# Performance work log

Hardware: AMD Instinct MI355X
Metric: run time of the kernel (lower is better)

## Reference

```python
import jax, jax.numpy as jnp
import numpy as np

N = 50000
E = 800000
F_IN = 128
HID = 64
HEADS = 4
EPS_BN = 1e-5
NEG_SLOPE = 0.2


def setup_inputs() -> dict:
    key = jax.random.key(0)
    ks = jax.random.split(key, 20)
    s = 0.05
    d = {
        "x": jax.random.normal(ks[0], (N, F_IN), jnp.float32),
        "edge_index": jax.random.randint(ks[1], (2, E), 0, N, dtype=jnp.int32),
        # layer 0: F_IN -> HID x HEADS (concat)
        "W0": jax.random.normal(ks[2], (F_IN, HEADS * HID), jnp.float32) * s,
        "as0": jax.random.normal(ks[3], (HEADS, HID), jnp.float32) * s,
        "ad0": jax.random.normal(ks[4], (HEADS, HID), jnp.float32) * s,
        "b0": jnp.zeros((HEADS * HID,), jnp.float32),
        # layer 1: HEADS*HID -> HID (heads=1)
        "W1": jax.random.normal(ks[5], (HEADS * HID, HID), jnp.float32) * s,
        "as1": jax.random.normal(ks[6], (1, HID), jnp.float32) * s,
        "ad1": jax.random.normal(ks[7], (1, HID), jnp.float32) * s,
        "b1": jnp.zeros((HID,), jnp.float32),
        # layer 2: HID -> HID (heads=1)
        "W2": jax.random.normal(ks[8], (HID, HID), jnp.float32) * s,
        "as2": jax.random.normal(ks[9], (1, HID), jnp.float32) * s,
        "ad2": jax.random.normal(ks[10], (1, HID), jnp.float32) * s,
        "b2": jnp.zeros((HID,), jnp.float32),
        # MLP head
        "lw1": jax.random.normal(ks[11], (HID, HID), jnp.float32) * s,
        "lb1": jnp.zeros((HID,), jnp.float32),
        "lw2": jax.random.normal(ks[12], (HID, 2), jnp.float32) * s,
        "lb2": jnp.zeros((2,), jnp.float32),
    }
    return d


def batch_norm(x):
    # track_running_stats=False, affine=False: per-batch stats, biased var
    mu = jnp.mean(x, axis=0)
    var = jnp.mean((x - mu) ** 2, axis=0)
    return (x - mu) / jnp.sqrt(var + EPS_BN)


def gat_conv(x, src, dst, W, att_src, att_dst, bias, heads, out_dim):
    n = x.shape[0]
    h = (x @ W).reshape(n, heads, out_dim)            # [N,H,D]
    a_src = jnp.sum(h * att_src, axis=-1)             # [N,H]
    a_dst = jnp.sum(h * att_dst, axis=-1)             # [N,H]
    e = a_src[src] + a_dst[dst]                       # [E',H]
    e = jax.nn.leaky_relu(e, NEG_SLOPE)
    # softmax over incoming edges of each destination node
    m = jax.ops.segment_max(e, dst, num_segments=n)   # [N,H]
    e = jnp.exp(e - m[dst])
    denom = jax.ops.segment_sum(e, dst, num_segments=n)
    alpha = e / (denom[dst] + 1e-16)                  # [E',H]
    msg = h[src] * alpha[:, :, None]                  # [E',H,D]
    out = jax.ops.segment_sum(msg, dst, num_segments=n)
    return out.reshape(n, heads * out_dim) + bias


def reference(x, edge_index, W0, as0, ad0, b0, W1, as1, ad1, b1,
              W2, as2, ad2, b2, lw1, lb1, lw2, lb2):
    n = x.shape[0]
    loop = jnp.arange(n, dtype=edge_index.dtype)
    src = jnp.concatenate([edge_index[0], loop])      # add self-loops (PyG default)
    dst = jnp.concatenate([edge_index[1], loop])

    h = gat_conv(x, src, dst, W0, as0, ad0, b0, HEADS, HID)
    h = jax.nn.relu(batch_norm(h))
    h = gat_conv(h, src, dst, W1, as1, ad1, b1, 1, HID)
    h = jax.nn.relu(batch_norm(h))
    h = gat_conv(h, src, dst, W2, as2, ad2, b2, 1, HID)
    h = jax.nn.relu(batch_norm(h))

    h = h @ lw1 + lb1
    h = jax.nn.relu(batch_norm(h))
    return h @ lw2 + lb2
```

## Files before the change

### kernel.cpp

```cpp
#include <hip/hip_runtime.h>

#define F_IN 128
#define EPS_BN 1e-5f
#define NCOPY 8

typedef __attribute__((ext_vector_type(8))) short short8v;
typedef __attribute__((ext_vector_type(4))) float f32x4;

__device__ __forceinline__ float lrelu(float x) { return x >= 0.f ? x : 0.2f * x; }
__device__ __forceinline__ unsigned short f2bf(float f) {
    unsigned int u = __float_as_uint(f);
    u += 0x7FFFu + ((u >> 16) & 1u);
    return (unsigned short)(u >> 16);
}
__device__ __forceinline__ float bf2f(unsigned short s) {
    return __uint_as_float(((unsigned int)s) << 16);
}

__global__ void k_deg(const int* __restrict__ ei, int e, int* __restrict__ deg) {
    int t = blockIdx.x * blockDim.x + threadIdx.x;
    if (t < e) atomicAdd(&deg[ei[e + t]], 1);
}

__global__ void k_offsets(const int* __restrict__ deg, int* __restrict__ startp,
                          int* __restrict__ cursor, int n) {
    int t = blockIdx.x * blockDim.x + threadIdx.x;
    int lane = threadIdx.x & 63;
    int da = (t < n) ? ((deg[t] + 7) & ~7) : 0;
    int pre = da;
    #pragma unroll
    for (int off = 1; off < 64; off <<= 1) {
        int u = __shfl_up(pre, off);
        if (lane >= off) pre += u;
    }
    int total = __shfl(pre, 63);
    int base = 0;
    if (lane == 0) base = atomicAdd(cursor, total);
    base = __shfl(base, 0);
    if (t < n) startp[t] = base + pre - da;
}

__global__ void k_fill(const int* __restrict__ ei, int e, const int* __restrict__ startp,
                       int* __restrict__ fill, int* __restrict__ col) {
    int t = blockIdx.x * blockDim.x + threadIdx.x;
    if (t < e) {
        int s = ei[t];
        int dd = ei[e + t];
        int p = startp[dd] + atomicAdd(&fill[dd], 1);
        col[p] = s;
    }
}

__global__ void k_pad(const int* __restrict__ startp, const int* __restrict__ deg,
                      int* __restrict__ col, int n) {
    int t = blockIdx.x * blockDim.x + threadIdx.x;
    if (t >= n) return;
    int s0 = startp[t], d = deg[t];
    int dpad = (d + 7) & ~7;
    for (int p = s0 + d; p < s0 + dpad; p++) col[p] = n;
}

__global__ void k_wprep_all(const float* __restrict__ W0, const float* __restrict__ W1,
                            const float* __restrict__ W2, const float* __restrict__ lw1,
                            const float* __restrict__ as0, const float* __restrict__ ad0,
                            unsigned short* __restrict__ Wt0, unsigned short* __restrict__ Wt1,
                            unsigned short* __restrict__ Wt2, unsigned short* __restrict__ Wtm,
                            float* __restrict__ vsd, float* __restrict__ a_src, int n)
{
    int t = blockIdx.x * blockDim.x + threadIdx.x;
    if (t < 32768) {
        int nn = t / 128, kk = t - nn * 128;
        Wt0[t] = f2bf(W0[(size_t)kk * 256 + nn]);
    } else if (t < 49152) {
        int u = t - 32768;
        int nn = u / 256, kk = u - nn * 256;
        Wt1[u] = f2bf(W1[(size_t)kk * 64 + nn]);
    } else if (t < 53248) {
        int u = t - 49152;
        int nn = u / 64, kk = u - nn * 64;
        Wt2[u] = f2bf(W2[(size_t)kk * 64 + nn]);
    } else if (t < 57344) {
        int u = t - 53248;
        int nn = u / 64, kk = u - nn * 64;
        Wtm[u] = f2bf(lw1[(size_t)kk * 64 + nn]);
    } else if (t < 57856) {
        int u = t - 57344;
        int h = u >> 7, k = u & 127;
        float s = 0.f;
        for (int d2 = 0; d2 < 64; d2++) s += W0[(size_t)k * 256 + h * 64 + d2] * as0[h * 64 + d2];
        vsd[u] = s;
    } else if (t < 58368) {
        int u = t - 57856;
        int h = u >> 7, k = u & 127;
        float s = 0.f;
        for (int d2 = 0; d2 < 64; d2++) s += W0[(size_t)k * 256 + h * 64 + d2] * ad0[h * 64 + d2];
        vsd[512 + u] = s;
    } else if (t < 58372) {
        a_src[4 * n + (t - 58368)] = -1e30f;
    }
}

__global__ void k_prep0(const float* __restrict__ x, const float* __restrict__ vsd,
                        unsigned short* __restrict__ xb,
                        float* __restrict__ a_src, float* __restrict__ a_dst, int n)
{
    int wv = (blockIdx.x * blockDim.x + threadIdx.x) >> 6;
    int lane = threadIdx.x & 63;
    if (wv >= n) return;
    const int xo = lane << 1;
    float2 xv = *reinterpret_cast<const float2*>(&x[(size_t)wv * 128 + xo]);
    ushort2 o;
    o.x = f2bf(xv.x); o.y = f2bf(xv.y);
    *reinterpret_cast<ushort2*>(&xb[(size_t)wv * 128 + xo]) = o;
    float ps[4], pd[4];
    #pragma unroll
    for (int h = 0; h < 4; h++) {
        float2 v2 = *reinterpret_cast<const float2*>(&vsd[h * 128 + xo]);
        float2 w2 = *reinterpret_cast<const float2*>(&vsd[512 + h * 128 + xo]);
        ps[h] = xv.x * v2.x + xv.y * v2.y;
        pd[h] = xv.x * w2.x + xv.y * w2.y;
    }
    #pragma unroll
    for (int off = 32; off; off >>= 1) {
        #pragma unroll
        for (int h = 0; h < 4; h++) {
            ps[h] += __shfl_xor(ps[h], off);
            pd[h] += __shfl_xor(pd[h], off);
        }
    }
    if (lane == 0) {
        *reinterpret_cast<float4*>(&a_src[wv * 4]) = make_float4(ps[0], ps[1], ps[2], ps[3]);
        *reinterpret_cast<float4*>(&a_dst[wv * 4]) = make_float4(pd[0], pd[1], pd[2], pd[3]);
    }
}

__global__ void k_aggx4(const unsigned short* __restrict__ xb,
                        const float* __restrict__ asrc, const float* __restrict__ adst,
                        const int* __restrict__ startp, const int* __restrict__ deg,
                        const int* __restrict__ col,
                        unsigned short* __restrict__ aggx, int n)
{
    __shared__ float lds_w[4][64];
    int wv = (blockIdx.x * blockDim.x + threadIdx.x) >> 6;
    int lane = threadIdx.x & 63;
    int wid = threadIdx.x >> 6;
    if (wv >= n) return;
    const int s0 = startp[wv], d = deg[wv];
    const int dpad = (d + 7) & ~7;
    const int eslot = (lane & 31) >> 2;
    const int hslot = lane & 3;
    const float4 adh4 = *reinterpret_cast<const float4*>(&adst[wv * 4]);
    const float4 asf4 = *reinterpret_cast<const float4*>(&asrc[wv * 4]);
    const float adh_h = hslot == 0 ? adh4.x : hslot == 1 ? adh4.y :
                        hslot == 2 ? adh4.z : adh4.w;
    const float w0 = __expf(lrelu(asf4.x + adh4.x));
    const float w1 = __expf(lrelu(asf4.y + adh4.y));
    const float w2 = __expf(lrelu(asf4.z + adh4.z));
    const float w3 = __expf(lrelu(asf4.w + adh4.w));
    const int xo = lane << 1;
    ushort2 xs = *reinterpret_cast<const ushort2*>(&xb[(size_t)wv * 128 + xo]);
    float x0 = bf2f(xs.x), x1 = bf2f(xs.y);
    float a00 = w0 * x0, a01 = w0 * x1;
    float a10 = w1 * x0, a11 = w1 * x1;
    float a20 = w2 * x0, a21 = w2 * x1;
    float a30 = w3 * x0, a31 = w3 * x1;
    float wsum = 0.f;
    const int* crow = col + s0;
    const float* asrcp = asrc + hslot;
    for (int t = 0; t < dpad; t += 8) {
        int se = crow[t + eslot];
        float wme = __expf(lrelu(asrcp[se * 4] + adh_h));
        wsum += wme;
        lds_w[wid][lane] = wme;
        int4 c0 = *reinterpret_cast<const int4*>(&crow[t]);
        int4 c1 = *reinterpret_cast<const int4*>(&crow[t + 4]);
        ushort2 uA = *reinterpret_cast<const ushort2*>(&xb[(size_t)c0.x * 128 + xo]);
        ushort2 uB = *reinterpret_cast<const ushort2*>(&xb[(size_t)c0.y * 128 + xo]);
        ushort2 uC = *reinterpret_cast<const ushort2*>(&xb[(size_t)c0.z * 128 + xo]);
        ushort2 uD = *reinterpret_cast<const ushort2*>(&xb[(size_t)c0.w * 128 + xo]);
        ushort2 uE = *reinterpret_cast<const ushort2*>(&xb[(size_t)c1.x * 128 + xo]);
        ushort2 uF = *reinterpret_cast<const ushort2*>(&xb[(size_t)c1.y * 128 + xo]);
        ushort2 uG = *reinterpret_cast<const ushort2*>(&xb[(size_t)c1.z * 128 + xo]);
        ushort2 uH = *reinterpret_cast<const ushort2*>(&xb[(size_t)c1.w * 128 + xo]);
        float4 wA = *reinterpret_cast<const float4*>(&lds_w[wid][0]);
        float4 wB = *reinterpret_cast<const float4*>(&lds_w[wid][4]);
        float4 wC = *reinterpret_cast<const float4*>(&lds_w[wid][8]);
        float4 wD = *reinterpret_cast<const float4*>(&lds_w[wid][12]);
        float4 wE = *reinterpret_cast<const float4*>(&lds_w[wid][16]);
        float4 wF = *reinterpret_cast<const float4*>(&lds_w[wid][20]);
        float4 wG = *reinterpret_cast<const float4*>(&lds_w[wid][24]);
        float4 wH = *reinterpret_cast<const float4*>(&lds_w[wid][28]);
        float xA0 = bf2f(uA.x), xA1 = bf2f(uA.y);
        float xB0 = bf2f(uB.x), xB1 = bf2f(uB.y);
        float xC0 = bf2f(uC.x), xC1 = bf2f(uC.y);
        float xD0 = bf2f(uD.x), xD1 = bf2f(uD.y);
        float xE0 = bf2f(uE.x), xE1 = bf2f(uE.y);
        float xF0 = bf2f(uF.x), xF1 = bf2f(uF.y);
        float xG0 = bf2f(uG.x), xG1 = bf2f(uG.y);
        float xH0 = bf2f(uH.x), xH1 = bf2f(uH.y);
        a00 += wA.x * xA0 + wB.x * xB0 + wC.x * xC0 + wD.x * xD0
             + wE.x * xE0 + wF.x * xF0 + wG.x * xG0 + wH.x * xH0;
        a01 += wA.x * xA1 + wB.x * xB1 + wC.x * xC1 + wD.x * xD1
             + wE.x * xE1 + wF.x * xF1 + wG.x * xG1 + wH.x * xH1;
        a10 += wA.y * xA0 + wB.y * xB0 + wC.y * xC0 + wD.y * xD0
             + wE.y * xE0 + wF.y * xF0 + wG.y * xG0 + wH.y * xH0;
        a11 += wA.y * xA1 + wB.y * xB1 + wC.y * xC1 + wD.y * xD1
             + wE.y * xE1 + wF.y * xF1 + wG.y * xG1 + wH.y * xH1;
        a20 += wA.z * xA0 + wB.z * xB0 + wC.z * xC0 + wD.z * xD0
             + wE.z * xE0 + wF.z * xF0 + wG.z * xG0 + wH.z * xH0;
        a21 += wA.z * xA1 + wB.z * xB1 + wC.z * xC1 + wD.z * xD1
             + wE.z * xE1 + wF.z * xF1 + wG.z * xG1 + wH.z * xH1;
        a30 += wA.w * xA0 + wB.w * xB0 + wC.w * xC0 + wD.w * xD0
             + wE.w * xE0 + wF.w * xF0 + wG.w * xG0 + wH.w * xH0;
        a31 += wA.w * xA1 + wB.w * xB1 + wC.w * xC1 + wD.w * xD1
             + wE.w * xE1 + wF.w * xF1 + wG.w * xG1 + wH.w * xH1;
    }
    wsum += __shfl_xor(wsum, 4);
    wsum += __shfl_xor(wsum, 8);
    wsum += __shfl_xor(wsum, 16);
    float r0 = 1.f / (w0 + __shfl(wsum, 0) + 1e-16f);
    float r1 = 1.f / (w1 + __shfl(wsum, 1) + 1e-16f);
    float r2 = 1.f / (w2 + __shfl(wsum, 2) + 1e-16f);
    float r3 = 1.f / (w3 + __shfl(wsum, 3) + 1e-16f);
    size_t base = (size_t)wv * 512 + xo;
    ushort2 o;
    o.x = f2bf(a00 * r0); o.y = f2bf(a01 * r0);
    *reinterpret_cast<ushort2*>(&aggx[base]) = o;
    o.x = f2bf(a10 * r1); o.y = f2bf(a11 * r1);
    *reinterpret_cast<ushort2*>(&aggx[base + 128]) = o;
    o.x = f2bf(a20 * r2); o.y = f2bf(a21 * r2);
    *reinterpret_cast<ushort2*>(&aggx[base + 256]) = o;
    o.x = f2bf(a30 * r3); o.y = f2bf(a31 * r3);
    *reinterpret_cast<ushort2*>(&aggx[base + 384]) = o;
}

__global__ __launch_bounds__(256) void k_gemm_bd(
    const unsigned short* __restrict__ Ab, const unsigned short* __restrict__ Wt,
    const float* __restrict__ bias, unsigned short* __restrict__ Cb0,
    float* __restrict__ ostats, int M)
{
    __shared__ unsigned short As[64 * 136];
    __shared__ unsigned short Bs[64 * 136];
    __shared__ float sred[4][4][16], sred2[4][4][16];
    const int tid = threadIdx.x;
    const int w = tid >> 6, lane = tid & 63;
    const int l15 = lane & 15, g = lane >> 4;
    const int bm = blockIdx.x * 64, bn = blockIdx.y * 64;
    const int hh = blockIdx.y;
    const int srow = tid >> 2;
    const int sk = (tid & 3) << 5;

    {
        short8v a0, a1, a2, a3;
        if (bm + srow < M) {
            const unsigned short* ap = &Ab[(size_t)(bm + srow) * 512 + hh * 128 + sk];
            a0 = *reinterpret_cast<const short8v*>(ap);
            a1 = *reinterpret_cast<const short8v*>(ap + 8);
            a2 = *reinterpret_cast<const short8v*>(ap + 16);
            a3 = *reinterpret_cast<const short8v*>(ap + 24);
        } else {
            a0 = a1 = a2 = a3 = (short8v){0,0,0,0,0,0,0,0};
        }
        const unsigned short* bp = &Wt[(size_t)(bn + srow) * 128 + sk];
        short8v b0v = *reinterpret_cast<const short8v*>(bp);
        short8v b1v = *reinterpret_cast<const short8v*>(bp + 8);
        short8v b2v = *reinterpret_cast<const short8v*>(bp + 16);
        short8v b3v = *reinterpret_cast<const short8v*>(bp + 24);
        unsigned short* arow = &As[srow * 136 + sk];
        *reinterpret_cast<short8v*>(arow) = a0;
        *reinterpret_cast<short8v*>(arow + 8) = a1;
        *reinterpret_cast<short8v*>(arow + 16) = a2;
        *reinterpret_cast<short8v*>(arow + 24) = a3;
        unsigned short* brow = &Bs[srow * 136 + sk];
        *reinterpret_cast<short8v*>(brow) = b0v;
        *reinterpret_cast<short8v*>(brow + 8) = b1v;
        *reinterpret_cast<short8v*>(brow + 16) = b2v;
        *reinterpret_cast<short8v*>(brow + 24) = b3v;
    }
    __syncthreads();

    f32x4 acc[4];
    #pragma unroll
    for (int nt = 0; nt < 4; nt++) acc[nt] = (f32x4){0.f, 0.f, 0.f, 0.f};
    #pragma unroll
    for (int kk = 0; kk < 4; kk++) {
        short8v af = *reinterpret_cast<const short8v*>(&As[(w * 16 + l15) * 136 + kk * 32 + g * 8]);
        #pragma unroll
        for (int nt = 0; nt < 4; nt++) {
            short8v bf = *reinterpret_cast<const short8v*>(&Bs[(nt * 16 + l15) * 136 + kk * 32 + g * 8]);
            acc[nt] = __builtin_amdgcn_mfma_f32_16x16x32_bf16(af, bf, acc[nt], 0, 0, 0);
        }
    }

    float s[4] = {0.f, 0.f, 0.f, 0.f}, s2[4] = {0.f, 0.f, 0.f, 0.f};
    #pragma unroll
    for (int reg = 0; reg < 4; reg++) {
        int row = bm + w * 16 + g * 4 + reg;
        if (row < M) {
            #pragma unroll
            for (int nt = 0; nt < 4; nt++) {
                float v = acc[nt][reg] + bias[bn + nt * 16 + l15];
                Cb0[(size_t)row * 256 + bn + nt * 16 + l15] = f2bf(v);
                s[nt] += v; s2[nt] += v * v;
            }
        }
    }
    #pragma unroll
    for (int off = 16; off <= 32; off <<= 1) {
        #pragma unroll
        for (int nt = 0; nt < 4; nt++) {
            s[nt]  += __shfl_xor(s[nt], off);
            s2[nt] += __shfl_xor(s2[nt], off);
        }
    }
    if (g == 0) {
        #pragma unroll
        for (int nt = 0; nt < 4; nt++) { sred[w][nt][l15] = s[nt]; sred2[w][nt][l15] = s2[nt]; }
    }
    __syncthreads();
    if (tid < 64) {
        int nt = tid >> 4, c = tid & 15;
        float S = 0.f, S2 = 0.f;
        #pragma unroll
        for (int w4 = 0; w4 < 4; w4++) { S += sred[w4][nt][c]; S2 += sred2[w4][nt][c]; }
        float* dst = ostats + (blockIdx.x & (NCOPY - 1)) * 512 + bn;
        atomicAdd(&dst[tid], S);
        atomicAdd(&dst[256 + tid], S2);
    }
}

template<bool BN, bool ATT, bool AB16>
__global__ __launch_bounds__(256) void k_gemm(
    const float* __restrict__ Af, const unsigned short* __restrict__ Abf,
    const unsigned short* __restrict__ Wt,
    const float* __restrict__ bias,
    const float* __restrict__ bnst, float invN,
    const float* __restrict__ att_s, const float* __restrict__ att_d,
    float* __restrict__ a_src, float* __restrict__ a_dst, int H,
    float* __restrict__ Cf, unsigned short* __restrict__ Cb,
    float* __restrict__ ostats,
    int M, int K, int Nc)
{
    __shared__ unsigned short As[64 * 40];
    __shared__ unsigned short Bs[64 * 40];
    __shared__ float muS[256], rsS[256];
    const int tid = threadIdx.x;
    const int w = tid >> 6, lane = tid & 63;
    const int l15 = lane & 15, g = lane >> 4;
    const int bm = blockIdx.x * 64, bn = blockIdx.y * 64;
    const int srow = tid >> 2;
    const int skq  = (tid & 3) << 3;

    if constexpr (BN) {
        if (tid < K) {
            float s = 0.f, s2 = 0.f;
            #pragma unroll
            for (int c = 0; c < NCOPY; c++) {
                s  += bnst[c * 2 * K + tid];
                s2 += bnst[c * 2 * K + K + tid];
            }
            float m = s * invN;
            float var = s2 * invN - m * m;
            muS[tid] = m;
            rsS[tid] = rsqrtf(var + EPS_BN);
        }
        __syncthreads();
    }

    f32x4 acc[4];
    #pragma unroll
    for (int nt = 0; nt < 4; nt++) acc[nt] = (f32x4){0.f, 0.f, 0.f, 0.f};

    for (int k0 = 0; k0 < K; k0 += 32) {
        short8v a8;
        if (bm + srow < M) {
            if constexpr (AB16) {
                short8v u = *reinterpret_cast<const short8v*>(&Abf[(size_t)(bm + srow) * K + k0 + skq]);
                if constexpr (BN) {
                    #pragma unroll
                    for (int j = 0; j < 8; j++) {
                        int kb = k0 + skq + j;
                        float f = bf2f((unsigned short)u[j]);
                        f = fmaxf((f - muS[kb]) * rsS[kb], 0.f);
                        a8[j] = (short)f2bf(f);
                    }
                } else {
                    a8 = u;
                }
            } else {
                const float* ap = &Af[(size_t)(bm + srow) * K + k0 + skq];
                float4 v0 = *reinterpret_cast<const float4*>(ap);
                float4 v1 = *reinterpret_cast<const float4*>(ap + 4);
                if constexpr (BN) {
                    int kb = k0 + skq;
                    v0.x = fmaxf((v0.x - muS[kb + 0]) * rsS[kb + 0], 0.f);
                    v0.y = fmaxf((v0.y - muS[kb + 1]) * rsS[kb + 1], 0.f);
                    v0.z = fmaxf((v0.z - muS[kb + 2]) * rsS[kb + 2], 0.f);
                    v0.w = fmaxf((v0.w - muS[kb + 3]) * rsS[kb + 3], 0.f);
                    v1.x = fmaxf((v1.x - muS[kb + 4]) * rsS[kb + 4], 0.f);
                    v1.y = fmaxf((v1.y - muS[kb + 5]) * rsS[kb + 5], 0.f);
                    v1.z = fmaxf((v1.z - muS[kb + 6]) * rsS[kb + 6], 0.f);
                    v1.w = fmaxf((v1.w - muS[kb + 7]) * rsS[kb + 7], 0.f);
                }
                a8[0] = (short)f2bf(v0.x); a8[1] = (short)f2bf(v0.y);
                a8[2] = (short)f2bf(v0.z); a8[3] = (short)f2bf(v0.w);
                a8[4] = (short)f2bf(v1.x); a8[5] = (short)f2bf(v1.y);
                a8[6] = (short)f2bf(v1.z); a8[7] = (short)f2bf(v1.w);
            }
        } else {
            a8 = (short8v){0,0,0,0,0,0,0,0};
        }
        short8v b8 = *reinterpret_cast<const short8v*>(&Wt[(size_t)(bn + srow) * K + k0 + skq]);
        __syncthreads();
        *reinterpret_cast<short8v*>(&As[srow * 40 + skq]) = a8;
        *reinterpret_cast<short8v*>(&Bs[srow * 40 + skq]) = b8;
        __syncthreads();
        short8v af = *reinterpret_cast<const short8v*>(&As[(w * 16 + l15) * 40 + g * 8]);
        #pragma unroll
        for (int nt = 0; nt < 4; nt++) {
            short8v bf = *reinterpret_cast<const short8v*>(&Bs[(nt * 16 + l15) * 40 + g * 8]);
            acc[nt] = __builtin_amdgcn_mfma_f32_16x16x32_bf16(af, bf, acc[nt], 0, 0, 0);
        }
    }

    if constexpr (ATT) {
        float wsv[4], wdv[4];
        #pragma unroll
        for (int nt = 0; nt < 4; nt++) {
            wsv[nt] = att_s[bn + nt * 16 + l15];
            wdv[nt] = att_d[bn + nt * 16 + l15];
        }
        #pragma unroll
        for (int reg = 0; reg < 4; reg++) {
            int row = bm + w * 16 + g * 4 + reg;
            float ps = 0.f, pd = 0.f;
            #pragma unroll
            for (int nt = 0; nt < 4; nt++) {
                float c = acc[nt][reg];
                ps += c * wsv[nt];
                pd += c * wdv[nt];
                if (row < M)
                    Cb[(size_t)row * Nc + bn + nt * 16 + l15] = f2bf(c);
            }
            #pragma unroll
            for (int off = 1; off < 16; off <<= 1) {
                ps += __shfl_xor(ps, off);
                pd += __shfl_xor(pd, off);
            }
            if (l15 == 0 && row < M) {
                int hh = bn >> 6;
                a_src[(size_t)row * H + hh] = ps;
                a_dst[(size_t)row * H + hh] = pd;
            }
        }
        if (H == 1 && blockIdx.x == 0 && blockIdx.y == 0 && tid == 0)
            a_src[M] = -1e30f;
    } else {
        __shared__ float sred[4][4][16], sred2[4][4][16];
        float s[4] = {0.f, 0.f, 0.f, 0.f}, s2[4] = {0.f, 0.f, 0.f, 0.f};
        #pragma unroll
        for (int reg = 0; reg < 4; reg++) {
            int row = bm + w * 16 + g * 4 + reg;
            if (row < M) {
                #pragma unroll
                for (int nt = 0; nt < 4; nt++) {
                    float v = acc[nt][reg] + bias[bn + nt * 16 + l15];
                    Cf[(size_t)row * Nc + bn + nt * 16 + l15] = v;
                    s[nt] += v; s2[nt] += v * v;
                }
            }
        }
        #pragma unroll
        for (int off = 16; off <= 32; off <<= 1) {
            #pragma unroll
            for (int nt = 0; nt < 4; nt++) {
                s[nt]  += __shfl_xor(s[nt], off);
                s2[nt] += __shfl_xor(s2[nt], off);
            }
        }
        if (g == 0) {
            #pragma unroll
            for (int nt = 0; nt < 4; nt++) { sred[w][nt][l15] = s[nt]; sred2[w][nt][l15] = s2[nt]; }
        }
        __syncthreads();
        if (tid < 64) {
            int nt = tid >> 4, c = tid & 15;
            float S = 0.f, S2 = 0.f;
            #pragma unroll
            for (int w4 = 0; w4 < 4; w4++) { S += sred[w4][nt][c]; S2 += sred2[w4][nt][c]; }
            float* dst = ostats + (blockIdx.x & (NCOPY - 1)) * 128;
            atomicAdd(&dst[tid], S);
            atomicAdd(&dst[64 + tid], S2);
        }
    }
}

__global__ void k_agg1f(const unsigned short* __restrict__ hb,
                        const float* __restrict__ asrc, const float* __restrict__ adst,
                        const int* __restrict__ startp, const int* __restrict__ deg,
                        const int* __restrict__ col, const float* __restrict__ bias,
                        float* __restrict__ out, float* __restrict__ ostats, int n)
{
    __shared__ float stage[4][64];
    int wv = (blockIdx.x * blockDim.x + threadIdx.x) >> 6;
    int lane = threadIdx.x & 63;
    int w = threadIdx.x >> 6;
    const int g = lane >> 4, l16 = lane & 15;
    float4 o = make_float4(0.f, 0.f, 0.f, 0.f);
    if (wv < n) {
        const int s0 = startp[wv], d = deg[wv];
        const int dpad = (d + 7) & ~7;
        const float adv = adst[wv];
        const size_t cb = (size_t)wv * 64 + (l16 << 2);
        float a0 = 0.f, a1 = 0.f, a2 = 0.f, a3 = 0.f, sm = 0.f;
        if (g == 0) {
            float ww = __expf(lrelu(asrc[wv] + adv));
            ushort4 v = *reinterpret_cast<const ushort4*>(&hb[cb]);
            a0 = ww * bf2f(v.x); a1 = ww * bf2f(v.y);
            a2 = ww * bf2f(v.z); a3 = ww * bf2f(v.w);
            sm = ww;
        }
        #pragma unroll 2
        for (int t = g; t < dpad; t += 4) {
            int s = col[s0 + t];
            float ww = __expf(lrelu(asrc[s] + adv));
            ushort4 u = *reinterpret_cast<const ushort4*>(&hb[(size_t)s * 64 + (l16 << 2)]);
            sm += ww;
            a0 += ww * bf2f(u.x); a1 += ww * bf2f(u.y);
            a2 += ww * bf2f(u.z); a3 += ww * bf2f(u.w);
        }
        #pragma unroll
        for (int off = 16; off <= 32; off <<= 1) {
            a0 += __shfl_xor(a0, off); a1 += __shfl_xor(a1, off);
            a2 += __shfl_xor(a2, off); a3 += __shfl_xor(a3, off);
            sm += __shfl_xor(sm, off);
        }
        if (g == 0) {
            float rv = 1.f / (sm + 1e-16f);
            float4 bv = *reinterpret_cast<const float4*>(&bias[l16 << 2]);
            o.x = a0 * rv + bv.x; o.y = a1 * rv + bv.y;
            o.z = a2 * rv + bv.z; o.w = a3 * rv + bv.w;
            *reinterpret_cast<float4*>(&out[cb]) = o;
        }
    }
    if (g == 0)
        *reinterpret_cast<float4*>(&stage[w][l16 << 2]) = o;
    __syncthreads();
    int tid = threadIdx.x;
    if (tid < 64) {
        float s = 0.f, s2 = 0.f;
        #pragma unroll
        for (int k = 0; k < 4; k++) {
            float v = stage[k][tid];
            s += v; s2 += v * v;
        }
        float* dst = ostats + (blockIdx.x & (NCOPY - 1)) * 128;
        atomicAdd(&dst[tid], s);
        atomicAdd(&dst[64 + tid], s2);
    }
}

__global__ void k_head(const float* __restrict__ h, const float* __restrict__ bnst,
                       float invN,
                       const float* __restrict__ lw2, const float* __restrict__ lb2,
                       float* __restrict__ out, int n)
{
    __shared__ float muH[64], rsH[64];
    int tid = threadIdx.x;
    if (tid < 64) {
        float s = 0.f, s2 = 0.f;
        #pragma unroll
        for (int c = 0; c < NCOPY; c++) {
            s  += bnst[c * 128 + tid];
            s2 += bnst[c * 128 + 64 + tid];
        }
        float m = s * invN;
        float var = s2 * invN - m * m;
        muH[tid] = m;
        rsH[tid] = rsqrtf(var + EPS_BN);
    }
    __syncthreads();
    int wv = (blockIdx.x * blockDim.x + threadIdx.x) >> 6;
    int lane = threadIdx.x & 63;
    if (wv >= n) return;
    float v = fmaxf((h[(size_t)wv * 64 + lane] - muH[lane]) * rsH[lane], 0.f);
    float c0 = v * lw2[lane * 2 + 0];
    float c1 = v * lw2[lane * 2 + 1];
    #pragma unroll
    for (int off = 32; off; off >>= 1) {
        c0 += __shfl_xor(c0, off);
        c1 += __shfl_xor(c1, off);
    }
    if (lane == 0) {
        out[wv * 2 + 0] = c0 + lb2[0];
        out[wv * 2 + 1] = c1 + lb2[1];
    }
}

extern "C" void kernel_launch(void* const* d_in, const int* in_sizes, int n_in,
                              void* d_out, int out_size, void* d_ws, size_t ws_size,
                              hipStream_t stream)
{
    const float* x   = (const float*)d_in[0];
    const int*   ei  = (const int*)d_in[1];
    const float* W0  = (const float*)d_in[2];
    const float* as0 = (const float*)d_in[3];
    const float* ad0 = (const float*)d_in[4];
    const float* b0  = (const float*)d_in[5];
    const float* W1  = (const float*)d_in[6];
    const float* as1 = (const float*)d_in[7];
    const float* ad1 = (const float*)d_in[8];
    const float* b1  = (const float*)d_in[9];
    const float* W2  = (const float*)d_in[10];
    const float* as2 = (const float*)d_in[11];
    const float* ad2 = (const float*)d_in[12];
    const float* b2  = (const float*)d_in[13];
    const float* lw1 = (const float*)d_in[14];
    const float* lb1 = (const float*)d_in[15];
    const float* lw2 = (const float*)d_in[16];
    const float* lb2 = (const float*)d_in[17];
    float* out = (float*)d_out;

    const int n = in_sizes[0] / F_IN;
    const int e = in_sizes[1] / 2;

    char* ws = (char*)d_ws;
    size_t off = 0;
    auto alloc = [&](size_t bytes) -> void* {
        void* p = ws + off;
        off += (bytes + 255) & ~(size_t)255;
        return p;
    };
    unsigned short* aggx = (unsigned short*)alloc((size_t)n * 512 * 2);
    unsigned short* Hb   = aggx;
    unsigned short* out0b = (unsigned short*)alloc((size_t)n * 256 * 2);
    float* B64 = (float*)alloc((size_t)n * 64 * 4);
    unsigned short* xb = (unsigned short*)alloc((size_t)(n + 1) * 128 * 2);
    float* g3 = (float*)xb;
    float* a_src = (float*)alloc(((size_t)n * 4 + 8) * 4);
    float* a_dst = (float*)alloc((size_t)n * 4 * 4);
    unsigned short* Wt0 = (unsigned short*)alloc(256 * 128 * 2);
    unsigned short* Wt1 = (unsigned short*)alloc(64 * 256 * 2);
    unsigned short* Wt2 = (unsigned short*)alloc(64 * 64 * 2);
    unsigned short* Wtm = (unsigned short*)alloc(64 * 64 * 2);
    float* vsd  = (float*)alloc(1024 * 4);
    int* col    = (int*)alloc(((size_t)e + 8 * (size_t)n) * 4);
    int* startp = (int*)alloc((size_t)n * 4);
    char* zbase = ws + off;
    float* st0 = (float*)alloc(NCOPY * 512 * 4);
    float* st1 = (float*)alloc(NCOPY * 128 * 4);
    float* st2 = (float*)alloc(NCOPY * 128 * 4);
    float* st3 = (float*)alloc(NCOPY * 128 * 4);
    int* deg    = (int*)alloc((size_t)n * 4);
    int* fill   = (int*)alloc((size_t)n * 4);
    int* cursor = (int*)alloc(256);
    size_t zsize = (size_t)((ws + off) - zbase);

    const float invN = 1.f / (float)n;

    hipMemsetAsync(zbase, 0, zsize, stream);

    const int tpb = 256;
    k_wprep_all<<<229, tpb, 0, stream>>>(W0, W1, W2, lw1, as0, ad0, Wt0, Wt1, Wt2, Wtm,
                                         vsd, a_src, n);

    k_deg<<<(e + tpb - 1) / tpb, tpb, 0, stream>>>(ei, e, deg);
    k_offsets<<<(n + tpb - 1) / tpb, tpb, 0, stream>>>(deg, startp, cursor, n);
    k_fill<<<(e + tpb - 1) / tpb, tpb, 0, stream>>>(ei, e, startp, fill, col);
    k_pad<<<(n + tpb - 1) / tpb, tpb, 0, stream>>>(startp, deg, col, n);

    const int wgrid = (n + 3) / 4;
    const int rowTiles = (n + 63) / 64;

    k_prep0<<<wgrid, 256, 0, stream>>>(x, vsd, xb, a_src, a_dst, n);
    k_aggx4<<<wgrid, 256, 0, stream>>>(xb, a_src, a_dst, startp, deg, col, aggx, n);
    k_gemm_bd<<<dim3(rowTiles, 4), 256, 0, stream>>>(aggx, Wt0, b0, out0b, st0, n);

    k_gemm<true, true, true><<<dim3(rowTiles, 1), 256, 0, stream>>>(
        nullptr, out0b, Wt1, nullptr, st0, invN, as1, ad1, a_src, a_dst, 1,
        nullptr, Hb, nullptr, n, 256, 64);
    k_agg1f<<<wgrid, 256, 0, stream>>>(Hb, a_src, a_dst, startp, deg, col, b1, B64, st1, n);

    k_gemm<true, true, false><<<dim3(rowTiles, 1), 256, 0, stream>>>(
        B64, nullptr, Wt2, nullptr, st1, invN, as2, ad2, a_src, a_dst, 1,
        nullptr, Hb, nullptr, n, 64, 64);
    k_agg1f<<<wgrid, 256, 0, stream>>>(Hb, a_src, a_dst, startp, deg, col, b2, B64, st2, n);

    k_gemm<true, false, false><<<dim3(rowTiles, 1), 256, 0, stream>>>(
        B64, nullptr, Wtm, lb1, st2, invN, nullptr, nullptr, nullptr, nullptr, 1,
        g3, nullptr, st3, n, 64, 64);

    k_head<<<wgrid, 256, 0, stream>>>(g3, st3, invN, lw2, lb2, out, n);
}
```

Measured before the change: 330.3 us.

## Build CSR via two-level bucket sort with shared-memory atomics

Replaces the global-atomic degree count, fill and pad kernels with a radix-style bucketing pass. Edges are histogrammed into 256-node bins per block and scattered as packed (dst,src) words. Per-bin kernels then count degrees and fill col using shared-memory atomics, and a single-block scan computes startp. The aim is less global atomic contention and better locality for the col writes, at the cost of more launches, a serial single-block scan, and 16-bit packing that only holds while n is at most 65536.

```diff
diff --git a/kernel.cpp b/kernel.cpp
--- a/kernel.cpp
+++ b/kernel.cpp
@@ -3,6 +3,7 @@
 #define F_IN 128
 #define EPS_BN 1e-5f
 #define NCOPY 8
+#define NBLK 512
 
 typedef __attribute__((ext_vector_type(8))) short short8v;
 typedef __attribute__((ext_vector_type(4))) float f32x4;
@@ -17,47 +18,124 @@
     return __uint_as_float(((unsigned int)s) << 16);
 }
 
-__global__ void k_deg(const int* __restrict__ ei, int e, int* __restrict__ deg) {
-    int t = blockIdx.x * blockDim.x + threadIdx.x;
-    if (t < e) atomicAdd(&deg[ei[e + t]], 1);
-}
-
-__global__ void k_offsets(const int* __restrict__ deg, int* __restrict__ startp,
-                          int* __restrict__ cursor, int n) {
-    int t = blockIdx.x * blockDim.x + threadIdx.x;
+
+__global__ void k_hist(const int* __restrict__ ei, int e, int* __restrict__ H, int nbin) {
+    __shared__ int hist[256];
+    int blk = blockIdx.x, tid = threadIdx.x;
+    if (tid < nbin) hist[tid] = 0;
+    __syncthreads();
+    int per = (e + NBLK - 1) / NBLK;
+    int t0 = blk * per, t1 = min(t0 + per, e);
+    for (int t = t0 + tid; t < t1; t += 256)
+        atomicAdd(&hist[ei[e + t] >> 8], 1);
+    __syncthreads();
+    if (tid < nbin) H[tid * NBLK + blk] = hist[tid];
+}
+
+__global__ void k_scanbins(const int* __restrict__ H, int* __restrict__ Hc,
+                           int* __restrict__ bintot, int nbin) {
+    int wv = (blockIdx.x * blockDim.x + threadIdx.x) >> 6;
     int lane = threadIdx.x & 63;
-    int da = (t < n) ? ((deg[t] + 7) & ~7) : 0;
-    int pre = da;
-    #pragma unroll
-    for (int off = 1; off < 64; off <<= 1) {
-        int u = __shfl_up(pre, off);
-        if (lane >= off) pre += u;
-    }
-    int total = __shfl(pre, 63);
-    int base = 0;
-    if (lane == 0) base = atomicAdd(cursor, total);
-    base = __shfl(base, 0);
-    if (t < n) startp[t] = base + pre - da;
-}
-
-__global__ void k_fill(const int* __restrict__ ei, int e, const int* __restrict__ startp,
-                       int* __restrict__ fill, int* __restrict__ col) {
-    int t = blockIdx.x * blockDim.x + threadIdx.x;
-    if (t < e) {
-        int s = ei[t];
-        int dd = ei[e + t];
-        int p = startp[dd] + atomicAdd(&fill[dd], 1);
-        col[p] = s;
-    }
-}
-
-__global__ void k_pad(const int* __restrict__ startp, const int* __restrict__ deg,
-                      int* __restrict__ col, int n) {
-    int t = blockIdx.x * blockDim.x + threadIdx.x;
-    if (t >= n) return;
-    int s0 = startp[t], d = deg[t];
-    int dpad = (d + 7) & ~7;
-    for (int p = s0 + d; p < s0 + dpad; p++) col[p] = n;
+    if (wv >= nbin) return;
+    int carry = 0;
+    for (int c = 0; c < NBLK; c += 64) {
+        int v = H[wv * NBLK + c + lane];
+        int s = v;
+        #pragma unroll
+        for (int off = 1; off < 64; off <<= 1) {
+            int u = __shfl_up(s, off);
+            if (lane >= off) s += u;
+        }
+        Hc[wv * NBLK + c + lane] = carry + s - v;
+        carry += __shfl(s, 63);
+    }
+    if (lane == 0) bintot[wv] = carry;
+}
+
+__global__ void k_scanbase(const int* __restrict__ bintot, int* __restrict__ SEbase, int nbin) {
+    __shared__ int buf[256];
+    int tid = threadIdx.x;
+    if (tid < nbin) buf[tid] = bintot[tid];
+    __syncthreads();
+    if (tid == 0) {
+        int run = 0;
+        for (int b = 0; b < nbin; b++) { SEbase[b] = run; run += buf[b]; }
+        SEbase[nbin] = run;
+    }
+}
+
+__global__ void k_scatter(const int* __restrict__ ei, int e, const int* __restrict__ Hc,
+                          const int* __restrict__ SEbase, unsigned int* __restrict__ SE, int nbin) {
+    __shared__ int cur[256];
+    int blk = blockIdx.x, tid = threadIdx.x;
+    if (tid < nbin) cur[tid] = SEbase[tid] + Hc[tid * NBLK + blk];
+    __syncthreads();
+    int per = (e + NBLK - 1) / NBLK;
+    int t0 = blk * per, t1 = min(t0 + per, e);
+    for (int t = t0 + tid; t < t1; t += 256) {
+        int s = ei[t], d = ei[e + t];
+        int pos = atomicAdd(&cur[d >> 8], 1);
+        SE[pos] = ((unsigned int)d << 16) | (unsigned int)s;
+    }
+}
+
+__global__ void k_degb(const unsigned int* __restrict__ SE, const int* __restrict__ SEbase,
+                       int* __restrict__ deg, int n) {
+    __shared__ int hist[256];
+    int b = blockIdx.x, tid = threadIdx.x;
+    hist[tid] = 0;
+    __syncthreads();
+    int t0 = SEbase[b], t1 = SEbase[b + 1];
+    for (int t = t0 + tid; t < t1; t += 256)
+        atomicAdd(&hist[(int)(SE[t] >> 16) - (b << 8)], 1);
+    __syncthreads();
+    int dst = (b << 8) + tid;
+    if (dst < n) deg[dst] = hist[tid];
+}
+
+__global__ __launch_bounds__(1024) void k_startp(const int* __restrict__ deg,
+                                                 int* __restrict__ startp, int n) {
+    __shared__ int part[1024];
+    int tid = threadIdx.x;
+    int chunk = (n + 1023) / 1024;
+    int i0 = tid * chunk, i1 = min(i0 + chunk, n);
+    int s = 0;
+    for (int i = i0; i < i1; i++) s += (deg[i] + 7) & ~7;
+    part[tid] = s;
+    __syncthreads();
+    for (int off = 1; off < 1024; off <<= 1) {
+        int v = (tid >= off) ? part[tid - off] : 0;
+        __syncthreads();
+        part[tid] += v;
+        __syncthreads();
+    }
+    int base = (tid == 0) ? 0 : part[tid - 1];
+    for (int i = i0; i < i1; i++) {
+        startp[i] = base;
+        base += (deg[i] + 7) & ~7;
+    }
+}
+
+__global__ void k_fillb(const unsigned int* __restrict__ SE, const int* __restrict__ SEbase,
+                        const int* __restrict__ startp, const int* __restrict__ deg,
+                        int* __restrict__ col, int n) {
+    __shared__ int cur[256];
+    int b = blockIdx.x, tid = threadIdx.x;
+    int dst = (b << 8) + tid;
+    cur[tid] = (dst < n) ? startp[dst] : 0;
+    __syncthreads();
+    int t0 = SEbase[b], t1 = SEbase[b + 1];
+    for (int t = t0 + tid; t < t1; t += 256) {
+        unsigned int se = SE[t];
+        int pos = atomicAdd(&cur[(int)(se >> 16) - (b << 8)], 1);
+        col[pos] = (int)(se & 0xFFFFu);
+    }
+    __syncthreads();
+    if (dst < n) {
+        int p = cur[tid];
+        int pe = startp[dst] + ((deg[dst] + 7) & ~7);
+        for (; p < pe; p++) col[p] = n;
+    }
 }
 
 __global__ void k_wprep_all(const float* __restrict__ W0, const float* __restrict__ W1,
@@ -623,6 +701,7 @@
 
     const int n = in_sizes[0] / F_IN;
     const int e = in_sizes[1] / 2;
+    const int nbin = (n + 255) >> 8;
 
     char* ws = (char*)d_ws;
     size_t off = 0;
@@ -633,7 +712,10 @@
     };
     unsigned short* aggx = (unsigned short*)alloc((size_t)n * 512 * 2);
     unsigned short* Hb   = aggx;
+    unsigned int*   SE   = (unsigned int*)aggx;
     unsigned short* out0b = (unsigned short*)alloc((size_t)n * 256 * 2);
+    int* H  = (int*)out0b;
+    int* Hc = (int*)(out0b + 512 * 1024);
     float* B64 = (float*)alloc((size_t)n * 64 * 4);
     unsigned short* xb = (unsigned short*)alloc((size_t)(n + 1) * 128 * 2);
     float* g3 = (float*)xb;
@@ -646,14 +728,14 @@
     float* vsd  = (float*)alloc(1024 * 4);
     int* col    = (int*)alloc(((size_t)e + 8 * (size_t)n) * 4);
     int* startp = (int*)alloc((size_t)n * 4);
+    int* deg    = (int*)alloc((size_t)n * 4);
+    int* bintot = (int*)alloc(512 * 4);
+    int* SEbase = (int*)alloc(512 * 4);
     char* zbase = ws + off;
     float* st0 = (float*)alloc(NCOPY * 512 * 4);
     float* st1 = (float*)alloc(NCOPY * 128 * 4);
     float* st2 = (float*)alloc(NCOPY * 128 * 4);
     float* st3 = (float*)alloc(NCOPY * 128 * 4);
-    int* deg    = (int*)alloc((size_t)n * 4);
-    int* fill   = (int*)alloc((size_t)n * 4);
-    int* cursor = (int*)alloc(256);
     size_t zsize = (size_t)((ws + off) - zbase);
 
     const float invN = 1.f / (float)n;
@@ -664,10 +746,13 @@
     k_wprep_all<<<229, tpb, 0, stream>>>(W0, W1, W2, lw1, as0, ad0, Wt0, Wt1, Wt2, Wtm,
                                          vsd, a_src, n);
 
-    k_deg<<<(e + tpb - 1) / tpb, tpb, 0, stream>>>(ei, e, deg);
-    k_offsets<<<(n + tpb - 1) / tpb, tpb, 0, stream>>>(deg, startp, cursor, n);
-    k_fill<<<(e + tpb - 1) / tpb, tpb, 0, stream>>>(ei, e, startp, fill, col);
-    k_pad<<<(n + tpb - 1) / tpb, tpb, 0, stream>>>(startp, deg, col, n);
+    k_hist<<<NBLK, tpb, 0, stream>>>(ei, e, H, nbin);
+    k_scanbins<<<(nbin * 64 + tpb - 1) / tpb, tpb, 0, stream>>>(H, Hc, bintot, nbin);
+    k_scanbase<<<1, tpb, 0, stream>>>(bintot, SEbase, nbin);
+    k_scatter<<<NBLK, tpb, 0, stream>>>(ei, e, Hc, SEbase, SE, nbin);
+    k_degb<<<nbin, tpb, 0, stream>>>(SE, SEbase, deg, n);
+    k_startp<<<1, 1024, 0, stream>>>(deg, startp, n);
+    k_fillb<<<nbin, tpb, 0, stream>>>(SE, SEbase, startp, deg, col, n);
 
     const int wgrid = (n + 3) / 4;
     const int rowTiles = (n + 63) / 64;
```

New measurement: 345.1 us. 1.04x slower.
